# Optimization experiments

Measured on AMD Instinct MI355X. Metric: run time of the kernel, lower is better.

The kernel has to match this reference:

```python
import jax, jax.numpy as jnp
import numpy as np

B, T, N, L = 128, 2048, 64, 256
NEG = -1e30  # safe -inf surrogate (avoids inf-inf NaNs in gradients)


def setup_inputs() -> dict:
    key = jax.random.key(0)
    k1, k2, k3, k4 = jax.random.split(key, 4)
    inputs = jax.random.normal(k1, (B, T, N), dtype=jnp.float32)
    target = jax.random.randint(k2, (B, L), 0, N, dtype=jnp.int32)
    # valid target lengths in [1, L]
    target_size = jax.random.randint(k3, (B,), 1, L + 1, dtype=jnp.int32)
    # module initializes trans to zeros; use small random values for a nontrivial reference
    trans = jax.random.normal(k4, (N, N), dtype=jnp.float32) * 0.1
    return {"input": inputs, "target": target, "target_size": target_size, "trans": trans}


def _fcc(inputs, trans):
    # Full-connection (partition) score: logsumexp over ALL label paths.
    # alpha_t[b, j] = input[b, t, j] + logsumexp_i( alpha_{t-1}[b, i] + trans[j, i] )
    def step(alpha, x_t):  # alpha: [B, N], x_t: [B, N]
        alpha = x_t + jax.nn.logsumexp(alpha[:, None, :] + trans[None, :, :], axis=2)
        return alpha, None

    alpha0 = inputs[:, 0, :]
    xs = jnp.swapaxes(inputs, 0, 1)[1:]  # [T-1, B, N]
    alphaT, _ = jax.lax.scan(step, alpha0, xs)
    return jax.nn.logsumexp(alphaT, axis=1)  # [B]


def _fac(inputs, trans, target, target_size):
    # Forced-alignment score: logsumexp over alignments emitting target labels
    # in order, each repeated >= 1 time (ASG: no blank).
    b = inputs.shape[0]
    b_idx = jnp.arange(b)
    trans_self = trans[target, target]                 # [B, L] stay on label l
    trans_move = trans[target[:, 1:], target[:, :-1]]  # [B, L-1] advance l-1 -> l
    neg_col = jnp.full((b, 1), NEG, dtype=inputs.dtype)

    alpha0 = jnp.full(target.shape, NEG, dtype=inputs.dtype)
    alpha0 = alpha0.at[:, 0].set(inputs[b_idx, 0, target[:, 0]])

    def step(alpha, x_t):  # alpha: [B, L], x_t: [B, N]
        emit = jnp.take_along_axis(x_t, target, axis=1)  # [B, L]
        stay = alpha + trans_self
        move = jnp.concatenate([neg_col, alpha[:, :-1] + trans_move], axis=1)
        alpha = emit + jnp.logaddexp(stay, move)
        return alpha, None

    xs = jnp.swapaxes(inputs, 0, 1)[1:]  # [T-1, B, N]
    alphaT, _ = jax.lax.scan(step, alpha0, xs)
    return alphaT[b_idx, target_size - 1]  # [B]


def reference(input, target, target_size, trans):
    # ASG loss = FullConnection (partition) - ForceAlignment (target score), per batch element.
    return _fcc(input, trans) - _fac(input, trans, target, target_size)
```

## Files before the change

### kernel.cpp

```cpp
#include <hip/hip_runtime.h>

#define B_ 128
#define T_ 2048
#define N_ 64
#define L_ 256
#define NEGV (-1e30f)
#define PITCH 72
#define LOG2E 1.4426950408889634f
#define LN2   0.6931471805599453f

typedef short  s16x4 __attribute__((ext_vector_type(4)));
typedef short  s16x8 __attribute__((ext_vector_type(8)));
typedef float  f32x4 __attribute__((ext_vector_type(4)));
typedef float  f32x16 __attribute__((ext_vector_type(16)));
typedef unsigned int u32x2 __attribute__((ext_vector_type(2)));
typedef unsigned int u32x4 __attribute__((ext_vector_type(4)));

__device__ __forceinline__ short f2bf_rne(float f) {
    unsigned u = __float_as_uint(f);
    unsigned r = (u + 0x7FFFu + ((u >> 16) & 1u)) >> 16;
    return (short)r;
}
__device__ __forceinline__ float bf2f(unsigned short u) {
    return __uint_as_float(((unsigned)u) << 16);
}
__device__ __forceinline__ float bperm(int byteaddr, float v) {
    return __int_as_float(__builtin_amdgcn_ds_bpermute(byteaddr, __float_as_int(v)));
}
__device__ __forceinline__ float ex2f(float x) { return __builtin_amdgcn_exp2f(x); }
__device__ __forceinline__ float lg2f(float x) { return __builtin_amdgcn_logf(x); }
__device__ __forceinline__ unsigned cvtpk_bf16(float lo, float hi) {
    unsigned r;
    asm("v_cvt_pk_bf16_f32 %0, %1, %2" : "=v"(r) : "v"(lo), "v"(hi));
    return r;
}
__device__ __forceinline__ void plswap32(unsigned &x, unsigned &y) {
    asm("v_permlane32_swap_b32 %0, %1" : "+v"(x), "+v"(y));
}

__global__ __launch_bounds__(256, 2) void asg_k1(
    const float* __restrict__ x,
    const int*   __restrict__ target,
    const int*   __restrict__ tsize,
    const float* __restrict__ trans,
    float* __restrict__ ws_c,
    unsigned short* __restrict__ ws_R,
    float* __restrict__ ws_v,
    float* __restrict__ ws_w)
{
    __shared__ float evbuf[4][N_];
    const int wid  = threadIdx.x >> 6;
    const int lane = threadIdx.x & 63;
    const int W    = blockIdx.x * 4 + wid;

    if (W < 128) {
        const int b  = W;
        const float* __restrict__ xb = x + (size_t)b * T_ * N_;
        const int l0 = lane * 4;
        int tga[4];
        float Sx0, Sx1, Sx2, Sx3, Mx0, Mx1, Mx2, Mx3;
        float al0, al1, al2, al3;
        {
            const int t0v = target[b * L_ + l0 + 0];
            const int t1v = target[b * L_ + l0 + 1];
            const int t2v = target[b * L_ + l0 + 2];
            const int t3v = target[b * L_ + l0 + 3];
            tga[0] = t0v << 2; tga[1] = t1v << 2;
            tga[2] = t2v << 2; tga[3] = t3v << 2;
            Sx0 = ex2f(trans[t0v * N_ + t0v] * LOG2E);
            Sx1 = ex2f(trans[t1v * N_ + t1v] * LOG2E);
            Sx2 = ex2f(trans[t2v * N_ + t2v] * LOG2E);
            Sx3 = ex2f(trans[t3v * N_ + t3v] * LOG2E);
            Mx1 = ex2f(trans[t1v * N_ + t0v] * LOG2E);
            Mx2 = ex2f(trans[t2v * N_ + t1v] * LOG2E);
            Mx3 = ex2f(trans[t3v * N_ + t2v] * LOG2E);
            const int tRm = target[b * L_ + ((l0 >= 1) ? l0 - 1 : 0)];
            Mx0 = ex2f(trans[t0v * N_ + tRm] * LOG2E);
            al0 = (lane == 0) ? xb[t0v] * LOG2E : NEGV;
            al1 = NEGV; al2 = NEGV; al3 = NEGV;
        }
        const int upA = ((lane == 0) ? 0 : lane - 1) << 2;

        float xr[16];
        #pragma unroll
        for (int i = 0; i < 16; ++i) xr[i] = xb[(size_t)(1 + i) * N_ + lane];
        float exn = ex2f(xr[0] * LOG2E);
        float ea0 = bperm(tga[0], exn), ea1 = bperm(tga[1], exn),
              ea2 = bperm(tga[2], exn), ea3 = bperm(tga[3], exn);
        exn = ex2f(xr[1] * LOG2E);
        float eb0 = bperm(tga[0], exn), eb1 = bperm(tga[1], exn),
              eb2 = bperm(tga[2], exn), eb3 = bperm(tga[3], exn);

        float A0, A1, A2, A3, mloc, cfm0;

        #define FPRO()                                                          \
        {                                                                       \
            float bpm_ = bperm(upA, al3);                                       \
            float ml_ = fmaxf(fmaxf(al0, al1), fmaxf(al2, al3));                \
            ml_ = fmaxf(ml_, bpm_);                                             \
            float mpl_ = bperm(upA, ml_);                                       \
            float cf_ = ex2f(fminf(mpl_ - ml_, 120.f));                         \
            cfm0 = (lane == 0) ? 0.f : cf_ * Mx0;                               \
            mloc = ml_;                                                         \
            A0 = ex2f(al0 - ml_); A1 = ex2f(al1 - ml_);                         \
            A2 = ex2f(al2 - ml_); A3 = ex2f(al3 - ml_);                         \
        }
        #define FEPI()                                                          \
        {                                                                       \
            al0 = fmaxf(lg2f(A0) + mloc, NEGV);                                 \
            al1 = fmaxf(lg2f(A1) + mloc, NEGV);                                 \
            al2 = fmaxf(lg2f(A2) + mloc, NEGV);                                 \
            al3 = fmaxf(lg2f(A3) + mloc, NEGV);                                 \
        }
        #define FSTEP(i, rp, RF, E0, E1, E2, E3)                                \
        {                                                                       \
            float A3bp = bperm(upA, A3);                                        \
            const float c0 = E0, c1 = E1, c2 = E2, c3 = E3;                     \
            float ex2_ = ex2f(xr[((i) + 2) & 15] * LOG2E);                      \
            E0 = bperm(tga[0], ex2_); E1 = bperm(tga[1], ex2_);                 \
            E2 = bperm(tga[2], ex2_); E3 = bperm(tga[3], ex2_);                 \
            if (RF) xr[i] = (rp)[lane];                                         \
            const float n0 = c0 * fmaf(A0, Sx0, A3bp * cfm0);                   \
            const float n1 = c1 * fmaf(A1, Sx1, A0 * Mx1);                      \
            const float n2 = c2 * fmaf(A2, Sx2, A1 * Mx2);                      \
            const float n3 = c3 * fmaf(A3, Sx3, A2 * Mx3);                      \
            A0 = n0; A1 = n1; A2 = n2; A3 = n3;                                 \
        }
        #define FPAIR(i, xp)                                                    \
            FSTEP(i, (xp) + (i) * N_, true, ea0, ea1, ea2, ea3)                 \
            FSTEP((i) + 1, (xp) + ((i) + 1) * N_, true, eb0, eb1, eb2, eb3)
        #define FPAIRX(i)                                                       \
            FSTEP(i, xb, false, ea0, ea1, ea2, ea3)                             \
            FSTEP((i) + 1, xb, false, eb0, eb1, eb2, eb3)

        for (int u = 0; u < 63; ++u) {
            const float* __restrict__ xp = xb + (size_t)(16 * u + 17) * N_;
            FPRO()
            FPAIR(0, xp) FPAIR(2, xp) FPAIR(4, xp) FPAIR(6, xp)
            FEPI()
            FPRO()
            FPAIR(8, xp) FPAIR(10, xp) FPAIR(12, xp) FPAIR(14, xp)
            FEPI()
        }
        FPRO()
        FPAIRX(0) FPAIRX(2) FPAIRX(4) FPAIRX(6)
        FEPI()
        FPRO()
        FPAIRX(8) FPAIRX(10) FPAIRX(12)
        FSTEP(14, xb, false, ea0, ea1, ea2, ea3)
        FEPI()
        #undef FSTEP
        #undef FPRO
        #undef FEPI
        #undef FPAIR
        #undef FPAIRX
        *(float4*)(ws_v + b * 256 + l0) = make_float4(al0, al1, al2, al3);
    } else if (W < 256) {
        const int b  = W - 128;
        const float* __restrict__ xb = x + (size_t)b * T_ * N_;
        const int l0 = lane * 4;
        const int lt = tsize[b] - 1;
        int tga[4], tgR;
        float Sx0, Sx1, Sx2, Sx3, Mx1, Mx2, Mx3, MRx;
        float al0, al1, al2, al3;
        {
            const int t0v = target[b * L_ + l0 + 0];
            const int t1v = target[b * L_ + l0 + 1];
            const int t2v = target[b * L_ + l0 + 2];
            const int t3v = target[b * L_ + l0 + 3];
            tga[0] = t0v << 2; tga[1] = t1v << 2;
            tga[2] = t2v << 2; tga[3] = t3v << 2;
            Sx0 = ex2f(trans[t0v * N_ + t0v] * LOG2E);
            Sx1 = ex2f(trans[t1v * N_ + t1v] * LOG2E);
            Sx2 = ex2f(trans[t2v * N_ + t2v] * LOG2E);
            Sx3 = ex2f(trans[t3v * N_ + t3v] * LOG2E);
            Mx1 = ex2f(trans[t1v * N_ + t0v] * LOG2E);
            Mx2 = ex2f(trans[t2v * N_ + t1v] * LOG2E);
            Mx3 = ex2f(trans[t3v * N_ + t2v] * LOG2E);
            const int tR = target[b * L_ + ((l0 + 4 <= L_ - 1) ? l0 + 4 : L_ - 1)];
            tgR = tR << 2;
            MRx = ex2f(trans[tR * N_ + t3v] * LOG2E);
            al0 = (l0 + 0 == lt) ? 0.f : NEGV;
            al1 = (l0 + 1 == lt) ? 0.f : NEGV;
            al2 = (l0 + 2 == lt) ? 0.f : NEGV;
            al3 = (l0 + 3 == lt) ? 0.f : NEGV;
        }
        const int dnA = ((lane == 63) ? 63 : lane + 1) << 2;

        float xr[16];
        #pragma unroll
        for (int i = 0; i < 16; ++i) xr[i] = xb[(size_t)(2047 - i) * N_ + lane];
        float exn = ex2f(xr[0] * LOG2E);
        float ea0 = bperm(tga[0], exn), ea1 = bperm(tga[1], exn),
              ea2 = bperm(tga[2], exn), ea3 = bperm(tga[3], exn),
              eaR = bperm(tgR, exn);
        exn = ex2f(xr[1] * LOG2E);
        float eb0 = bperm(tga[0], exn), eb1 = bperm(tga[1], exn),
              eb2 = bperm(tga[2], exn), eb3 = bperm(tga[3], exn),
              ebR = bperm(tgR, exn);

        float A0, A1, A2, A3, mloc, cfm;

        #define BPRO()                                                          \
        {                                                                       \
            float bpm_ = bperm(dnA, al0);                                       \
            float ml_ = fmaxf(fmaxf(al0, al1), fmaxf(al2, al3));                \
            ml_ = fmaxf(ml_, bpm_);                                             \
            float mpl_ = bperm(dnA, ml_);                                       \
            float cf_ = ex2f(fminf(mpl_ - ml_, 120.f));                         \
            cfm = (lane == 63) ? 0.f : cf_ * MRx;                               \
            mloc = ml_;                                                         \
            A0 = ex2f(al0 - ml_); A1 = ex2f(al1 - ml_);                         \
            A2 = ex2f(al2 - ml_); A3 = ex2f(al3 - ml_);                         \
        }
        #define BEPI()                                                          \
        {                                                                       \
            al0 = fmaxf(lg2f(A0) + mloc, NEGV);                                 \
            al1 = fmaxf(lg2f(A1) + mloc, NEGV);                                 \
            al2 = fmaxf(lg2f(A2) + mloc, NEGV);                                 \
            al3 = fmaxf(lg2f(A3) + mloc, NEGV);                                 \
        }
        #define BSTEP(i, rp, RF, E0, E1, E2, E3, ER)                            \
        {                                                                       \
            float A0bp = bperm(dnA, A0);                                        \
            const float c0 = E0, c1 = E1, c2 = E2, c3 = E3, cR = ER;            \
            float ex2_ = ex2f(xr[((i) + 2) & 15] * LOG2E);                      \
            E0 = bperm(tga[0], ex2_); E1 = bperm(tga[1], ex2_);                 \
            E2 = bperm(tga[2], ex2_); E3 = bperm(tga[3], ex2_);                 \
            ER = bperm(tgR, ex2_);                                              \
            if (RF) xr[i] = (rp)[lane];                                         \
            const float T0 = A0 * c0, T1 = A1 * c1, T2 = A2 * c2, T3 = A3 * c3; \
            const float n0 = fmaf(T1, Mx1, T0 * Sx0);                           \
            const float n1 = fmaf(T2, Mx2, T1 * Sx1);                           \
            const float n2 = fmaf(T3, Mx3, T2 * Sx2);                           \
            const float n3 = fmaf(A0bp * cR, cfm, T3 * Sx3);                    \
            A0 = n0; A1 = n1; A2 = n2; A3 = n3;                                 \
        }
        #define BPAIR(i, xp)                                                    \
            BSTEP(i, (xp) - (size_t)(i) * N_, true, ea0, ea1, ea2, ea3, eaR)    \
            BSTEP((i) + 1, (xp) - (size_t)((i) + 1) * N_, true, eb0, eb1, eb2, eb3, ebR)
        #define BPAIRX(i)                                                       \
            BSTEP(i, xb, false, ea0, ea1, ea2, ea3, eaR)                        \
            BSTEP((i) + 1, xb, false, eb0, eb1, eb2, eb3, ebR)

        for (int u = 0; u < 63; ++u) {
            const float* __restrict__ xp = xb + (size_t)(2047 - 16 * u - 16) * N_;
            BPRO()
            BPAIR(0, xp) BPAIR(2, xp) BPAIR(4, xp) BPAIR(6, xp)
            BEPI()
            BPRO()
            BPAIR(8, xp) BPAIR(10, xp) BPAIR(12, xp) BPAIR(14, xp)
            BEPI()
        }
        BPRO()
        BPAIRX(0) BPAIRX(2) BPAIRX(4) BPAIRX(6)
        BEPI()
        BPRO()
        BPAIRX(8) BPAIRX(10) BPAIRX(12) BPAIRX(14)
        BEPI()
        #undef BSTEP
        #undef BPRO
        #undef BEPI
        #undef BPAIR
        #undef BPAIRX
        *(float4*)(ws_w + b * 256 + l0) = make_float4(al0, al1, al2, al3);
    } else {
        const int task = W - 256;
        const int b = task >> 5, k = task & 31;
        const int lane31 = lane & 31, hi = lane >> 5;
        const float* __restrict__ xb = x + (size_t)b * T_ * N_;
        const int t0 = k * 64;
        float* __restrict__ evb = evbuf[wid];

        s16x8 Ahat[2][4];
        float rsum[2];
        #pragma unroll
        for (int r = 0; r < 2; ++r) {
            float rs = 0.f;
            const float* tp = trans + (32 * r + lane31) * N_;
            #pragma unroll
            for (int kt = 0; kt < 4; ++kt) {
                const float* tq = tp + 16 * kt + 8 * hi;
                float4 ta = *(const float4*)tq;
                float4 tb = *(const float4*)(tq + 4);
                float v0 = __expf(ta.x), v1 = __expf(ta.y),
                      v2 = __expf(ta.z), v3 = __expf(ta.w);
                float v4 = __expf(tb.x), v5 = __expf(tb.y),
                      v6 = __expf(tb.z), v7 = __expf(tb.w);
                s16x8 af;
                af[0] = f2bf_rne(v0); af[1] = f2bf_rne(v1);
                af[2] = f2bf_rne(v2); af[3] = f2bf_rne(v3);
                af[4] = f2bf_rne(v4); af[5] = f2bf_rne(v5);
                af[6] = f2bf_rne(v6); af[7] = f2bf_rne(v7);
                rs += ((v0 + v1) + (v2 + v3)) + ((v4 + v5) + (v6 + v7));
                Ahat[r][kt] = af;
            }
            rsum[r] = rs;
        }
        rsum[0] += __shfl_xor(rsum[0], 32);
        rsum[1] += __shfl_xor(rsum[1], 32);
        float rmax = fmaxf(rsum[0], rsum[1]);
        #pragma unroll
        for (int o = 16; o > 0; o >>= 1) rmax = fmaxf(rmax, __shfl_xor(rmax, o));
        const float LS = __logf(rmax);

        s16x8 Pf[4][2];
        #pragma unroll
        for (int kt = 0; kt < 4; ++kt)
            #pragma unroll
            for (int c = 0; c < 2; ++c) {
                s16x8 pf;
                #pragma unroll
                for (int j = 0; j < 8; ++j)
                    pf[j] = (16 * kt + 8 * hi + j == 32 * c + lane31)
                              ? (short)0x3F80 : (short)0;
                Pf[kt][c] = pf;
            }

        const f32x16 z16 = {};
        f32x16 Y00 = {}, Y01 = {}, Y10 = {}, Y11 = {};
        float xpre[4];
        #pragma unroll
        for (int d = 0; d < 4; ++d)
            xpre[d] = xb[(size_t)(t0 + 1 + d) * N_ + lane];
        float c_acc = 0.f;

        #define MM(af, bf, cf) __builtin_amdgcn_mfma_f32_32x32x16_bf16(af, bf, cf, 0, 0, 0)
        #define REDIST(kt, c, Yv)                                               \
        {                                                                       \
            unsigned P0 = cvtpk_bf16(Yv[8*((kt)&1) + 0], Yv[8*((kt)&1) + 1]);   \
            unsigned P1 = cvtpk_bf16(Yv[8*((kt)&1) + 2], Yv[8*((kt)&1) + 3]);   \
            unsigned Q0 = cvtpk_bf16(Yv[8*((kt)&1) + 4], Yv[8*((kt)&1) + 5]);   \
            unsigned Q1 = cvtpk_bf16(Yv[8*((kt)&1) + 6], Yv[8*((kt)&1) + 7]);   \
            plswap32(P0, Q0); plswap32(P1, Q1);                                 \
            u32x4 uv; uv[0] = P0; uv[1] = P1; uv[2] = Q0; uv[3] = Q1;           \
            Pf[kt][c] = __builtin_bit_cast(s16x8, uv);                          \
        }

        #pragma unroll 1
        for (int u = 0; u < 16; ++u) {
            #pragma unroll
            for (int i = 0; i < 4; ++i) {
                const int s = 4 * u + i;
                const int t = t0 + 1 + s;
                if (t < T_) {
                    const float xt = xpre[i];
                    int tp2 = t + 4; if (tp2 > T_ - 1) tp2 = T_ - 1;
                    xpre[i] = xb[(size_t)tp2 * N_ + lane];
                    const float gt = __uint_as_float(
                        __builtin_amdgcn_readfirstlane(__float_as_uint(xt))) + LS;
                    c_acc += gt;
                    evb[lane] = __expf(xt - gt);
                    float4 E[2][4];
                    #pragma unroll
                    for (int r = 0; r < 2; ++r)
                        #pragma unroll
                        for (int q = 0; q < 4; ++q)
                            E[r][q] = *(const float4*)&evb[32 * r + 8 * q + 4 * hi];
                    Y00 = MM(Ahat[0][0], Pf[0][0], z16);
                    Y01 = MM(Ahat[0][0], Pf[0][1], z16);
                    Y10 = MM(Ahat[1][0], Pf[0][0], z16);
                    Y11 = MM(Ahat[1][0], Pf[0][1], z16);
                    #pragma unroll
                    for (int kt = 1; kt < 4; ++kt) {
                        Y00 = MM(Ahat[0][kt], Pf[kt][0], Y00);
                        Y01 = MM(Ahat[0][kt], Pf[kt][1], Y01);
                        Y10 = MM(Ahat[1][kt], Pf[kt][0], Y10);
                        Y11 = MM(Ahat[1][kt], Pf[kt][1], Y11);
                    }
                    #pragma unroll
                    for (int q = 0; q < 4; ++q) {
                        Y00[4*q+0] *= E[0][q].x; Y00[4*q+1] *= E[0][q].y;
                        Y00[4*q+2] *= E[0][q].z; Y00[4*q+3] *= E[0][q].w;
                        Y01[4*q+0] *= E[0][q].x; Y01[4*q+1] *= E[0][q].y;
                        Y01[4*q+2] *= E[0][q].z; Y01[4*q+3] *= E[0][q].w;
                        Y10[4*q+0] *= E[1][q].x; Y10[4*q+1] *= E[1][q].y;
                        Y10[4*q+2] *= E[1][q].z; Y10[4*q+3] *= E[1][q].w;
                        Y11[4*q+0] *= E[1][q].x; Y11[4*q+1] *= E[1][q].y;
                        Y11[4*q+2] *= E[1][q].z; Y11[4*q+3] *= E[1][q].w;
                    }
                    REDIST(0, 0, Y00); REDIST(0, 1, Y01);
                    REDIST(1, 0, Y00); REDIST(1, 1, Y01);
                    REDIST(2, 0, Y10); REDIST(2, 1, Y11);
                    REDIST(3, 0, Y10); REDIST(3, 1, Y11);
                }
            }
        }
        #undef REDIST
        #undef MM

        unsigned short* dst = ws_R + (size_t)(b * 32 + k) * 4096;
        #pragma unroll
        for (int q = 0; q < 4; ++q)
            #pragma unroll
            for (int m = 0; m < 4; ++m) {
                const int reg = 4 * q + m;
                const int rw  = 8 * q + 4 * hi + m;
                dst[(rw     ) * 64 + lane31     ] = (unsigned short)f2bf_rne(Y00[reg]);
                dst[(rw     ) * 64 + 32 + lane31] = (unsigned short)f2bf_rne(Y01[reg]);
                dst[(32 + rw) * 64 + lane31     ] = (unsigned short)f2bf_rne(Y10[reg]);
                dst[(32 + rw) * 64 + 32 + lane31] = (unsigned short)f2bf_rne(Y11[reg]);
            }
        if (lane == 0) ws_c[b * 32 + k] = c_acc;
    }
}

__global__ __launch_bounds__(128) void asg_k2(
    const float* __restrict__ x,
    const float* __restrict__ ws_c,
    const unsigned short* __restrict__ ws_R,
    const float* __restrict__ ws_v,
    const float* __restrict__ ws_w,
    float* __restrict__ out)
{
    __shared__ short rb[2][N_ * PITCH];
    __shared__ __align__(16) float sa[N_];
    __shared__ float sres[2];
    const int b = blockIdx.x, tid = threadIdx.x, lane = tid & 63;

    if (tid < 64) {
        float a0 = x[(size_t)b * T_ * N_ + lane];
        float m0 = a0;
        #pragma unroll
        for (int o = 32; o > 0; o >>= 1) m0 = fmaxf(m0, __shfl_xor(m0, o));
        float  a  = __expf(a0 - m0);
        double Cd = (double)m0;

        const unsigned short* Rb = ws_R + (size_t)b * 32 * 4096;
        const int frow = (lane >> 3), fcol = (lane & 7) * 8;
        {
            #pragma unroll
            for (int q = 0; q < 8; ++q) {
                s16x8 v = *(const s16x8*)(Rb + lane * 8 + 512 * q);
                *(s16x8*)&rb[0][(frow + 8 * q) * PITCH + fcol] = v;
            }
        }
        s16x8 nvA[8], nvB[8];
        #pragma unroll
        for (int q = 0; q < 8; ++q)
            nvA[q] = *(const s16x8*)(Rb + (size_t)4096 + lane * 8 + 512 * q);

        auto k2_step = [&](int kk, int bufi) {
            sa[lane] = a;
            float4 sav[16];
            #pragma unroll
            for (int q = 0; q < 16; ++q) sav[q] = ((const float4*)sa)[q];
            float acc4[4] = {0.f, 0.f, 0.f, 0.f};
            #pragma unroll
            for (int u = 0; u < 8; ++u) {
                s16x8 rr = *(const s16x8*)&rb[bufi][lane * PITCH + u * 8];
                const float4 s0 = sav[2 * u], s1 = sav[2 * u + 1];
                acc4[0] = fmaf(bf2f((unsigned short)rr[0]), s0.x, acc4[0]);
                acc4[1] = fmaf(bf2f((unsigned short)rr[1]), s0.y, acc4[1]);
                acc4[2] = fmaf(bf2f((unsigned short)rr[2]), s0.z, acc4[2]);
                acc4[3] = fmaf(bf2f((unsigned short)rr[3]), s0.w, acc4[3]);
                acc4[0] = fmaf(bf2f((unsigned short)rr[4]), s1.x, acc4[0]);
                acc4[1] = fmaf(bf2f((unsigned short)rr[5]), s1.y, acc4[1]);
                acc4[2] = fmaf(bf2f((unsigned short)rr[6]), s1.z, acc4[2]);
                acc4[3] = fmaf(bf2f((unsigned short)rr[7]), s1.w, acc4[3]);
            }
            float acc = (acc4[0] + acc4[1]) + (acc4[2] + acc4[3]);
            float rm = acc;
            #pragma unroll
            for (int o = 32; o > 0; o >>= 1) rm = fmaxf(rm, __shfl_xor(rm, o));
            a = acc / rm;
            Cd += (double)(__logf(rm) + ws_c[b * 32 + kk]);
        };

        for (int kk = 0; kk < 32; kk += 2) {
            const int kA = (kk + 2 < 32) ? kk + 2 : 31;
            #pragma unroll
            for (int q = 0; q < 8; ++q)
                nvB[q] = *(const s16x8*)(Rb + (size_t)kA * 4096 + lane * 8 + 512 * q);
            k2_step(kk, kk & 1);
            #pragma unroll
            for (int q = 0; q < 8; ++q)
                *(s16x8*)&rb[(kk + 1) & 1][(frow + 8 * q) * PITCH + fcol] = nvA[q];
            const int kB = (kk + 3 < 32) ? kk + 3 : 31;
            #pragma unroll
            for (int q = 0; q < 8; ++q)
                nvA[q] = *(const s16x8*)(Rb + (size_t)kB * 4096 + lane * 8 + 512 * q);
            k2_step(kk + 1, (kk + 1) & 1);
            #pragma unroll
            for (int q = 0; q < 8; ++q)
                *(s16x8*)&rb[kk & 1][(frow + 8 * q) * PITCH + fcol] = nvB[q];
        }
        float ssum = a;
        #pragma unroll
        for (int o = 32; o > 0; o >>= 1) ssum += __shfl_xor(ssum, o);
        if (lane == 0) sres[0] = (float)(Cd + (double)__logf(ssum));
    } else {
        float4 v4 = ((const float4*)(ws_v + b * 256))[lane];
        float4 w4 = ((const float4*)(ws_w + b * 256))[lane];
        const float s0 = v4.x + w4.x, s1 = v4.y + w4.y,
                    s2 = v4.z + w4.z, s3 = v4.w + w4.w;
        float m = fmaxf(fmaxf(s0, s1), fmaxf(s2, s3));
        #pragma unroll
        for (int o = 32; o > 0; o >>= 1) m = fmaxf(m, __shfl_xor(m, o));
        float sum = __builtin_amdgcn_exp2f(s0 - m) + __builtin_amdgcn_exp2f(s1 - m)
                  + __builtin_amdgcn_exp2f(s2 - m) + __builtin_amdgcn_exp2f(s3 - m);
        #pragma unroll
        for (int o = 32; o > 0; o >>= 1) sum += __shfl_xor(sum, o);
        if (lane == 0) sres[1] = (m + __builtin_amdgcn_logf(sum)) * LN2;
    }
    __syncthreads();
    if (tid == 0) out[b] = sres[0] - sres[1];
}

extern "C" void kernel_launch(void* const* d_in, const int* in_sizes, int n_in,
                              void* d_out, int out_size, void* d_ws, size_t ws_size,
                              hipStream_t stream) {
    (void)in_sizes; (void)n_in; (void)out_size; (void)ws_size;
    const float* xin    = (const float*)d_in[0];
    const int*   target = (const int*)  d_in[1];
    const int*   tsz    = (const int*)  d_in[2];
    const float* trans  = (const float*)d_in[3];
    float* out = (float*)d_out;

    float*          ws_c = (float*)d_ws;
    unsigned short* ws_R = (unsigned short*)((char*)d_ws + 16384);
    float*          ws_v = (float*)((char*)d_ws + 16384 + 33554432);
    float*          ws_w = (float*)((char*)d_ws + 16384 + 33554432 + 131072);

    asg_k1<<<dim3(1088), dim3(256), 0, stream>>>(xin, target, tsz, trans,
                                                 ws_c, ws_R, ws_v, ws_w);
    asg_k2<<<dim3(B_), dim3(128), 0, stream>>>(xin, ws_c, ws_R, ws_v, ws_w, out);
}
```

Baseline: 245.9 us.

## Pair forward and backward alignment waves per block, simplify chain prefetch

The wave-to-task mapping in the first kernel changes. Each of the first 128 blocks now runs the forward and backward alignment recurrences for the same batch element on waves 0 and 1, and its other two waves take chunk-transfer tasks. This spreads the long serial alignment waves across more blocks and compute units instead of packing them into the first 64 blocks. In the second kernel, the two-step unrolled double-buffered prefetch of the bf16 transfer matrices becomes a simpler one-ahead prefetch per step, which shortens the prefetch distance but lowers register pressure.

```diff
diff --git a/kernel.cpp b/kernel.cpp
--- a/kernel.cpp
+++ b/kernel.cpp
@@ -51,10 +51,11 @@
     __shared__ float evbuf[4][N_];
     const int wid  = threadIdx.x >> 6;
     const int lane = threadIdx.x & 63;
-    const int W    = blockIdx.x * 4 + wid;
-
-    if (W < 128) {
-        const int b  = W;
+    const int bx   = blockIdx.x;
+    const bool lowblk = (bx < 128);
+
+    if (lowblk && wid == 0) {
+        const int b  = bx;
         const float* __restrict__ xb = x + (size_t)b * T_ * N_;
         const int l0 = lane * 4;
         int tga[4];
@@ -155,8 +156,8 @@
         #undef FPAIR
         #undef FPAIRX
         *(float4*)(ws_v + b * 256 + l0) = make_float4(al0, al1, al2, al3);
-    } else if (W < 256) {
-        const int b  = W - 128;
+    } else if (lowblk && wid == 1) {
+        const int b  = bx;
         const float* __restrict__ xb = x + (size_t)b * T_ * N_;
         const int l0 = lane * 4;
         const int lt = tsize[b] - 1;
@@ -265,7 +266,8 @@
         #undef BPAIRX
         *(float4*)(ws_w + b * 256 + l0) = make_float4(al0, al1, al2, al3);
     } else {
-        const int task = W - 256;
+        const int task = lowblk ? (bx * 2 + (wid - 2))
+                                : (256 + (bx - 128) * 4 + wid);
         const int b = task >> 5, k = task & 31;
         const int lane31 = lane & 31, hi = lane >> 5;
         const float* __restrict__ xb = x + (size_t)b * T_ * N_;
@@ -435,20 +437,22 @@
                 *(s16x8*)&rb[0][(frow + 8 * q) * PITCH + fcol] = v;
             }
         }
-        s16x8 nvA[8], nvB[8];
-        #pragma unroll
-        for (int q = 0; q < 8; ++q)
-            nvA[q] = *(const s16x8*)(Rb + (size_t)4096 + lane * 8 + 512 * q);
-
-        auto k2_step = [&](int kk, int bufi) {
+        for (int kk = 0; kk < 32; ++kk) {
+            const int kn = (kk < 31) ? kk + 1 : 31;
+            s16x8 nv[8];
+            #pragma unroll
+            for (int q = 0; q < 8; ++q)
+                nv[q] = *(const s16x8*)(Rb + (size_t)kn * 4096 + lane * 8 + 512 * q);
+
             sa[lane] = a;
             float4 sav[16];
             #pragma unroll
             for (int q = 0; q < 16; ++q) sav[q] = ((const float4*)sa)[q];
+
             float acc4[4] = {0.f, 0.f, 0.f, 0.f};
             #pragma unroll
             for (int u = 0; u < 8; ++u) {
-                s16x8 rr = *(const s16x8*)&rb[bufi][lane * PITCH + u * 8];
+                s16x8 rr = *(const s16x8*)&rb[kk & 1][lane * PITCH + u * 8];
                 const float4 s0 = sav[2 * u], s1 = sav[2 * u + 1];
                 acc4[0] = fmaf(bf2f((unsigned short)rr[0]), s0.x, acc4[0]);
                 acc4[1] = fmaf(bf2f((unsigned short)rr[1]), s0.y, acc4[1]);
@@ -465,25 +469,10 @@
             for (int o = 32; o > 0; o >>= 1) rm = fmaxf(rm, __shfl_xor(rm, o));
             a = acc / rm;
             Cd += (double)(__logf(rm) + ws_c[b * 32 + kk]);
-        };
-
-        for (int kk = 0; kk < 32; kk += 2) {
-            const int kA = (kk + 2 < 32) ? kk + 2 : 31;
+
             #pragma unroll
             for (int q = 0; q < 8; ++q)
-                nvB[q] = *(const s16x8*)(Rb + (size_t)kA * 4096 + lane * 8 + 512 * q);
-            k2_step(kk, kk & 1);
-            #pragma unroll
-            for (int q = 0; q < 8; ++q)
-                *(s16x8*)&rb[(kk + 1) & 1][(frow + 8 * q) * PITCH + fcol] = nvA[q];
-            const int kB = (kk + 3 < 32) ? kk + 3 : 31;
-            #pragma unroll
-            for (int q = 0; q < 8; ++q)
-                nvA[q] = *(const s16x8*)(Rb + (size_t)kB * 4096 + lane * 8 + 512 * q);
-            k2_step(kk + 1, (kk + 1) & 1);
-            #pragma unroll
-            for (int q = 0; q < 8; ++q)
-                *(s16x8*)&rb[kk & 1][(frow + 8 * q) * PITCH + fcol] = nvB[q];
+                *(s16x8*)&rb[(kk + 1) & 1][(frow + 8 * q) * PITCH + fcol] = nv[q];
         }
         float ssum = a;
         #pragma unroll
```

Measured after the change: 246.6 us. Within noise of the previous version (+0.3%).
